# Kernel optimization log

Measured on AMD Instinct MI355X. Metric: run time of the kernel, lower is better.

## Reference

```python
import jax, jax.numpy as jnp
import numpy as np

GROUP_SIZE = 16
MIN_SIGMA = 1e-4


def setup_inputs() -> dict:
    key = jax.random.key(0)
    k1, k2, k3 = jax.random.split(key, 3)
    B, N, M, F = 4, 8192, 4096, 64
    return {
        "point_cloud": jax.random.normal(k1, (B, 3, N), dtype=jnp.float32),
        "query_cloud": jax.random.normal(k2, (B, 3, M), dtype=jnp.float32),
        "point_features": jax.random.normal(k3, (B, F, N), dtype=jnp.float32),
        "temperature": jnp.asarray(1.0, dtype=jnp.float32),
    }


def reference(point_cloud, query_cloud, point_features, temperature):
    # point_cloud: (B,3,N), query_cloud: (B,3,M), point_features: (B,F,N)
    k = GROUP_SIZE
    # Pairwise squared distances (B, M, N): ||q||^2 + ||p||^2 - 2 q.p
    q_sq = jnp.sum(query_cloud ** 2, axis=1)              # (B, M)
    p_sq = jnp.sum(point_cloud ** 2, axis=1)              # (B, N)
    qp = jnp.einsum('bdm,bdn->bmn', query_cloud, point_cloud)
    d2 = q_sq[:, :, None] + p_sq[:, None, :] - 2.0 * qp   # (B, M, N)
    # k nearest neighbors per query
    _, idx = jax.lax.top_k(-d2, k)                         # (B, M, k)

    # Gather neighbor coords and features: (B, 3, M, k), (B, F, M, k)
    idx_b = idx[:, None, :, :]                             # (B,1,M,k)
    grouped_points = jnp.take_along_axis(
        point_cloud[:, :, None, :], jnp.broadcast_to(idx_b, (idx.shape[0], 3, idx.shape[1], k)), axis=3)
    grouped_features = jnp.take_along_axis(
        point_features[:, :, None, :],
        jnp.broadcast_to(idx_b, (idx.shape[0], point_features.shape[1], idx.shape[1], k)), axis=3)

    # Soft-projection weights
    sigma = jnp.maximum(temperature ** 2, jnp.asarray(MIN_SIGMA, dtype=temperature.dtype))
    deltas = grouped_points - query_cloud[:, :, :, None]   # (B,3,M,k)
    dist = jnp.sum(deltas ** 2, axis=1, keepdims=True) / sigma  # (B,1,M,k)
    weights = jax.nn.softmax(-dist, axis=3)                # (B,1,M,k)

    projected_points = jnp.sum(grouped_points * weights, axis=3)     # (B,3,M)
    propagated_features = jnp.sum(grouped_features * weights, axis=3)  # (B,F,M)
    return (projected_points, propagated_features)
```

## Files before the change

kernel.cpp:

```cpp
#include <hip/hip_runtime.h>


#define BB 4
#define NN 8192
#define MM 4096
#define FF 64
#define KK 16
#define CHUNK 2048
#define NCHUNK 4
#define QPW 4
#define QPB 32
#define SCAP 54
#define NTHR 1024
#define STG 33

__device__ __forceinline__ float min3f(float a, float b, float c) {
    float d;
    asm("v_min3_f32 %0, %1, %2, %3" : "=v"(d) : "v"(a), "v"(b), "v"(c));
    return d;
}

__global__ __launch_bounds__(256) void transpose_feat(const float* __restrict__ pf,
                                                      float* __restrict__ pfT) {
    __shared__ float tile[64][65];
    const int b = blockIdx.y;
    const int n0 = blockIdx.x * 64;
    const int t = threadIdx.x;
    const int n = t & 63, fq = t >> 6;
#pragma unroll
    for (int i = 0; i < 16; ++i) {
        int f = fq * 16 + i;
        tile[f][n] = pf[(size_t)b * FF * NN + (size_t)f * NN + n0 + n];
    }
    __syncthreads();
    const int f2 = t & 63, nq = t >> 6;
#pragma unroll
    for (int i = 0; i < 16; ++i) {
        int nn2 = nq * 16 + i;
        pfT[(size_t)b * NN * FF + (size_t)(n0 + nn2) * FF + f2] = tile[f2][nn2];
    }
}

__device__ __forceinline__ unsigned mapf(float f) {
    unsigned u = __float_as_uint(f);
    return (u & 0x80000000u) ? ~u : (u | 0x80000000u);
}
__device__ __forceinline__ float unmapf(unsigned k) {
    return (k & 0x80000000u) ? __uint_as_float(k ^ 0x80000000u)
                             : __uint_as_float(~k);
}

#define STAGE(C)                                                            \
    do {                                                                    \
        if (t < CHUNK / 4) {                                                \
            int base_ = (C)*CHUNK + t * 4;                                  \
            float4 x4_ = *(const float4*)(pcb + base_);                     \
            float4 y4_ = *(const float4*)(pcb + NN + base_);                \
            float4 z4_ = *(const float4*)(pcb + 2 * NN + base_);            \
            *(float4*)(s_pts + t * 4) = x4_;                                \
            *(float4*)(s_pts + CHUNK + t * 4) = y4_;                        \
            *(float4*)(s_pts + 2 * CHUNK + t * 4) = z4_;                    \
            float4 p4_;                                                     \
            p4_.x = fmaf(x4_.x, x4_.x, fmaf(y4_.x, y4_.x, z4_.x * z4_.x));  \
            p4_.y = fmaf(x4_.y, x4_.y, fmaf(y4_.y, y4_.y, z4_.y * z4_.y));  \
            p4_.z = fmaf(x4_.z, x4_.z, fmaf(y4_.z, y4_.z, z4_.z * z4_.z));  \
            p4_.w = fmaf(x4_.w, x4_.w, fmaf(y4_.w, y4_.w, z4_.w * z4_.w));  \
            *(float4*)(s_pts + 3 * CHUNK + t * 4) = p4_;                    \
        }                                                                   \
    } while (0)

#define VAL(X, Y, Z, PS, QX, QY, QZ) \
    fmaf((X), (QX), fmaf((Y), (QY), fmaf((Z), (QZ), (PS))))

#define PUSH(WQ, V, I)                                          \
    do {                                                        \
        int pos_ = atomicAdd(&s_cnt[WQ], 1);                    \
        if (pos_ < SCAP) {                                      \
            s_surv[((WQ)*SCAP + pos_) * 2] = (V);               \
            s_surv[((WQ)*SCAP + pos_) * 2 + 1] = __int_as_float(I); \
        }                                                       \
    } while (0)

__global__ __launch_bounds__(NTHR, 8) void soft_proj_kernel(
    const float* __restrict__ pc, const float* __restrict__ qc,
    const float* __restrict__ pf, const float* __restrict__ pfT,
    const float* __restrict__ temp, float* __restrict__ out, int useT) {
    __shared__ __align__(16) float s_pts[4 * CHUNK];
    __shared__ __align__(16) float s_surv[QPB * SCAP * 2];
    __shared__ int s_cnt[QPB];
    __shared__ int s_sel[QPB * KK];
    __shared__ float s_thr[2 * QPB];

    const int bid = blockIdx.x;
    const int b = bid >> 7;
    const int m0 = (bid & 127) * QPB;
    const int t = threadIdx.x;
    const int wave = t >> 6;
    const int lane = t & 63;
    const int pairIdx = wave & 7;
    const int half = wave >> 3;

    const float* pcb = pc + (size_t)b * 3 * NN;
    const float* qcb = qc + (size_t)b * 3 * MM;

    float qx2[QPW], qy2[QPW], qz2[QPW];
#pragma unroll
    for (int q = 0; q < QPW; ++q) {
        int m = m0 + pairIdx * QPW + q;
        qx2[q] = -2.0f * qcb[m];
        qy2[q] = -2.0f * qcb[MM + m];
        qz2[q] = -2.0f * qcb[2 * MM + m];
    }

    float mnA[QPW], mnB[QPW];
#pragma unroll
    for (int q = 0; q < QPW; ++q) { mnA[q] = 3.0e38f; mnB[q] = 3.0e38f; }

    for (int c = 0; c < NCHUNK; ++c) {
        __syncthreads();
        STAGE(c);
        __syncthreads();
        const int ob = half * 1024 + lane * 4;
#pragma unroll
        for (int g = 0; g < 4; ++g) {
            int oo = ob + g * 256;
            float4 x4 = *(const float4*)(s_pts + oo);
            float4 y4 = *(const float4*)(s_pts + CHUNK + oo);
            float4 z4 = *(const float4*)(s_pts + 2 * CHUNK + oo);
            float4 p4 = *(const float4*)(s_pts + 3 * CHUNK + oo);
#pragma unroll
            for (int q = 0; q < QPW; ++q) {
                float v0 = VAL(x4.x, y4.x, z4.x, p4.x, qx2[q], qy2[q], qz2[q]);
                float v1 = VAL(x4.y, y4.y, z4.y, p4.y, qx2[q], qy2[q], qz2[q]);
                float v2 = VAL(x4.z, y4.z, z4.z, p4.z, qx2[q], qy2[q], qz2[q]);
                float v3 = VAL(x4.w, y4.w, z4.w, p4.w, qx2[q], qy2[q], qz2[q]);
                mnA[q] = min3f(v0, v1, mnA[q]);
                mnB[q] = min3f(v2, v3, mnB[q]);
            }
        }
    }

#pragma unroll
    for (int q = 0; q < QPW; ++q) {
        unsigned key = mapf(fminf(mnA[q], mnB[q]));
        unsigned res = 0u;
        for (int bb = 31; bb >= 16; --bb) {
            unsigned cand = res | (1u << bb);
            unsigned long long bal = __ballot(key < cand);
            int c2 = __popcll(bal);
            if (c2 < 8) res = cand;
        }
        if (lane == 0)
            s_thr[half * QPB + pairIdx * QPW + q] = unmapf(res | 0xFFFFu);
    }
    if (t < QPB) s_cnt[t] = 0;
    __syncthreads();

    const int qo = (wave >> 2) * 8;
    const int qtr = wave & 3;
    float qx2b[8], qy2b[8], qz2b[8], thv[8];
#pragma unroll
    for (int q = 0; q < 8; ++q) {
        int m = m0 + qo + q;
        qx2b[q] = -2.0f * qcb[m];
        qy2b[q] = -2.0f * qcb[MM + m];
        qz2b[q] = -2.0f * qcb[2 * MM + m];
        thv[q] = fmaxf(s_thr[qo + q], s_thr[QPB + qo + q]);
    }

    for (int c = 0; c < NCHUNK; ++c) {
        __syncthreads();
        STAGE(c);
        __syncthreads();
        const int ob = qtr * 512 + lane * 4;
#pragma unroll
        for (int g = 0; g < 2; ++g) {
            int oo = ob + g * 256;
            float4 x4 = *(const float4*)(s_pts + oo);
            float4 y4 = *(const float4*)(s_pts + CHUNK + oo);
            float4 z4 = *(const float4*)(s_pts + 2 * CHUNK + oo);
            float4 p4 = *(const float4*)(s_pts + 3 * CHUNK + oo);
            int gi = c * CHUNK + oo;
#pragma unroll
            for (int q = 0; q < 8; ++q) {
                float v0 = VAL(x4.x, y4.x, z4.x, p4.x, qx2b[q], qy2b[q], qz2b[q]);
                float v1 = VAL(x4.y, y4.y, z4.y, p4.y, qx2b[q], qy2b[q], qz2b[q]);
                float v2 = VAL(x4.z, y4.z, z4.z, p4.z, qx2b[q], qy2b[q], qz2b[q]);
                float v3 = VAL(x4.w, y4.w, z4.w, p4.w, qx2b[q], qy2b[q], qz2b[q]);
                if (fminf(min3f(v0, v1, v2), v3) <= thv[q]) {
                    int wqq = qo + q;
                    if (v0 <= thv[q]) PUSH(wqq, v0, gi + 0);
                    if (v1 <= thv[q]) PUSH(wqq, v1, gi + 1);
                    if (v2 <= thv[q]) PUSH(wqq, v2, gi + 2);
                    if (v3 <= thv[q]) PUSH(wqq, v3, gi + 3);
                }
            }
        }
    }
    __syncthreads();

#pragma unroll
    for (int qq = 0; qq < 2; ++qq) {
        int wq = wave * 2 + qq;
        int cnt = s_cnt[wq];
        cnt = __builtin_amdgcn_readfirstlane(cnt);
        if (cnt > SCAP) cnt = SCAP;
        bool valid = lane < cnt;
        float mv = 0.f;
        int mi = 0;
        if (valid) {
            mv = s_surv[(wq * SCAP + lane) * 2];
            mi = __float_as_int(s_surv[(wq * SCAP + lane) * 2 + 1]);
        }
        int rank = 0;
        for (int j = 0; j < cnt; ++j) {
            float vj = s_surv[(wq * SCAP + j) * 2];
            int ij = __float_as_int(s_surv[(wq * SCAP + j) * 2 + 1]);
            if (valid && (vj < mv || (vj == mv && ij < mi))) rank++;
        }
        if (valid && rank < KK) s_sel[wq * KK + rank] = mi;
    }
    __syncthreads();

    float* stage = s_surv;
    float tval = temp[0];
    float sigma = fmaxf(tval * tval, 1.0e-4f);
    float inv_sigma = 1.0f / sigma;
    const float* pfTb = pfT + (size_t)b * NN * FF;
    const float* pfb = pf + (size_t)b * FF * NN;

#pragma unroll
    for (int qq = 0; qq < 2; ++qq) {
        int wq = wave * 2 + qq;
        int m = m0 + wq;
        float qxe = qcb[m], qye = qcb[MM + m], qze = qcb[2 * MM + m];
        int ik = s_sel[wq * KK + (lane & 15)];
        float px = pcb[ik], py = pcb[NN + ik], pz = pcb[2 * NN + ik];
        float dx = px - qxe, dy = py - qye, dz = pz - qze;
        float dk = fmaf(dx, dx, fmaf(dy, dy, dz * dz));
        float dmin = dk;
#pragma unroll
        for (int s = 1; s < 16; s <<= 1) dmin = fminf(dmin, __shfl_xor(dmin, s));
        float e = __expf((dmin - dk) * inv_sigma);
        float ssum = e;
#pragma unroll
        for (int s = 1; s < 16; s <<= 1) ssum += __shfl_xor(ssum, s);
        float w = e * (1.0f / ssum);
        float sx = w * px, sy = w * py, sz = w * pz;
#pragma unroll
        for (int s = 1; s < 16; s <<= 1) {
            sx += __shfl_xor(sx, s);
            sy += __shfl_xor(sy, s);
            sz += __shfl_xor(sz, s);
        }
        float facc = 0.f;
#pragma unroll
        for (int k = 0; k < KK; ++k) {
            float wk = __shfl(w, k);
            int iik = __shfl(ik, k);
            float fv = useT ? pfTb[(size_t)iik * FF + lane]
                            : pfb[(size_t)lane * NN + iik];
            facc = fmaf(wk, fv, facc);
        }
        stage[lane * STG + wq] = facc;
        if (lane == 0) {
            stage[(64) * STG + wq] = sx;
            stage[(65) * STG + wq] = sy;
            stage[(66) * STG + wq] = sz;
        }
    }
    __syncthreads();

    const size_t featOff = (size_t)BB * 3 * MM;
    for (int j = t; j < 67 * QPB; j += NTHR) {
        int row = j >> 5, col = j & 31;
        float v = stage[row * STG + col];
        int m = m0 + col;
        if (row < 64)
            out[featOff + (size_t)b * FF * MM + (size_t)row * MM + m] = v;
        else
            out[(size_t)b * 3 * MM + (size_t)(row - 64) * MM + m] = v;
    }
}

extern "C" void kernel_launch(void* const* d_in, const int* in_sizes, int n_in,
                              void* d_out, int out_size, void* d_ws, size_t ws_size,
                              hipStream_t stream) {
    (void)in_sizes; (void)n_in; (void)out_size;
    const float* pc = (const float*)d_in[0];
    const float* qc = (const float*)d_in[1];
    const float* pf = (const float*)d_in[2];
    const float* temp = (const float*)d_in[3];
    float* out = (float*)d_out;
    float* pfT = (float*)d_ws;
    const size_t needT = (size_t)BB * NN * FF * sizeof(float);
    int useT = (ws_size >= needT && d_ws != nullptr) ? 1 : 0;

    if (useT) {
        hipLaunchKernelGGL(transpose_feat, dim3(NN / 64, BB), dim3(256), 0, stream,
                           pf, pfT);
    }
    hipLaunchKernelGGL(soft_proj_kernel, dim3((BB * MM) / QPB), dim3(NTHR), 0,
                       stream, pc, qc, pf, pfT, temp, out, useT);
}
```

Baseline: 137.0 us.

## Stage full-width point chunks and reuse pass-one query mapping in survivor pass

Doubles the shared-memory chunk to 4096 points so all 1024 threads stage data, halving the number of staging rounds and barriers in both passes. The second (survivor-collection) pass now reuses the first pass's query-to-wave mapping and register-held query coordinates, so the extra loads and the 8-query layout are gone. s_sel is aliased onto s_pts to offset the larger shared buffer. The trade-off is more LDS per block, which may lower occupancy, and fewer queries per wave in pass two, which means more shared-memory point reads per query.

```diff
diff --git a/kernel.cpp b/kernel.cpp
--- a/kernel.cpp
+++ b/kernel.cpp
@@ -6,8 +6,8 @@
 #define MM 4096
 #define FF 64
 #define KK 16
-#define CHUNK 2048
-#define NCHUNK 4
+#define CHUNK 4096
+#define NCHUNK 2
 #define QPW 4
 #define QPB 32
 #define SCAP 54
@@ -52,21 +52,19 @@
 
 #define STAGE(C)                                                            \
     do {                                                                    \
-        if (t < CHUNK / 4) {                                                \
-            int base_ = (C)*CHUNK + t * 4;                                  \
-            float4 x4_ = *(const float4*)(pcb + base_);                     \
-            float4 y4_ = *(const float4*)(pcb + NN + base_);                \
-            float4 z4_ = *(const float4*)(pcb + 2 * NN + base_);            \
-            *(float4*)(s_pts + t * 4) = x4_;                                \
-            *(float4*)(s_pts + CHUNK + t * 4) = y4_;                        \
-            *(float4*)(s_pts + 2 * CHUNK + t * 4) = z4_;                    \
-            float4 p4_;                                                     \
-            p4_.x = fmaf(x4_.x, x4_.x, fmaf(y4_.x, y4_.x, z4_.x * z4_.x));  \
-            p4_.y = fmaf(x4_.y, x4_.y, fmaf(y4_.y, y4_.y, z4_.y * z4_.y));  \
-            p4_.z = fmaf(x4_.z, x4_.z, fmaf(y4_.z, y4_.z, z4_.z * z4_.z));  \
-            p4_.w = fmaf(x4_.w, x4_.w, fmaf(y4_.w, y4_.w, z4_.w * z4_.w));  \
-            *(float4*)(s_pts + 3 * CHUNK + t * 4) = p4_;                    \
-        }                                                                   \
+        int base_ = (C)*CHUNK + t * 4;                                      \
+        float4 x4_ = *(const float4*)(pcb + base_);                         \
+        float4 y4_ = *(const float4*)(pcb + NN + base_);                    \
+        float4 z4_ = *(const float4*)(pcb + 2 * NN + base_);                \
+        *(float4*)(s_pts + t * 4) = x4_;                                    \
+        *(float4*)(s_pts + CHUNK + t * 4) = y4_;                            \
+        *(float4*)(s_pts + 2 * CHUNK + t * 4) = z4_;                        \
+        float4 p4_;                                                         \
+        p4_.x = fmaf(x4_.x, x4_.x, fmaf(y4_.x, y4_.x, z4_.x * z4_.x));      \
+        p4_.y = fmaf(x4_.y, x4_.y, fmaf(y4_.y, y4_.y, z4_.y * z4_.y));      \
+        p4_.z = fmaf(x4_.z, x4_.z, fmaf(y4_.z, y4_.z, z4_.z * z4_.z));      \
+        p4_.w = fmaf(x4_.w, x4_.w, fmaf(y4_.w, y4_.w, z4_.w * z4_.w));      \
+        *(float4*)(s_pts + 3 * CHUNK + t * 4) = p4_;                        \
     } while (0)
 
 #define VAL(X, Y, Z, PS, QX, QY, QZ) \
@@ -88,8 +86,8 @@
     __shared__ __align__(16) float s_pts[4 * CHUNK];
     __shared__ __align__(16) float s_surv[QPB * SCAP * 2];
     __shared__ int s_cnt[QPB];
-    __shared__ int s_sel[QPB * KK];
     __shared__ float s_thr[2 * QPB];
+    int* s_sel = (int*)s_pts;
 
     const int bid = blockIdx.x;
     const int b = bid >> 7;
@@ -120,9 +118,9 @@
         __syncthreads();
         STAGE(c);
         __syncthreads();
-        const int ob = half * 1024 + lane * 4;
-#pragma unroll
-        for (int g = 0; g < 4; ++g) {
+        const int ob = half * 2048 + lane * 4;
+#pragma unroll
+        for (int g = 0; g < 8; ++g) {
             int oo = ob + g * 256;
             float4 x4 = *(const float4*)(s_pts + oo);
             float4 y4 = *(const float4*)(s_pts + CHUNK + oo);
@@ -155,26 +153,18 @@
     }
     if (t < QPB) s_cnt[t] = 0;
     __syncthreads();
-
-    const int qo = (wave >> 2) * 8;
-    const int qtr = wave & 3;
-    float qx2b[8], qy2b[8], qz2b[8], thv[8];
-#pragma unroll
-    for (int q = 0; q < 8; ++q) {
-        int m = m0 + qo + q;
-        qx2b[q] = -2.0f * qcb[m];
-        qy2b[q] = -2.0f * qcb[MM + m];
-        qz2b[q] = -2.0f * qcb[2 * MM + m];
-        thv[q] = fmaxf(s_thr[qo + q], s_thr[QPB + qo + q]);
-    }
+    float thv[QPW];
+#pragma unroll
+    for (int q = 0; q < QPW; ++q)
+        thv[q] = fmaxf(s_thr[pairIdx * QPW + q], s_thr[QPB + pairIdx * QPW + q]);
 
     for (int c = 0; c < NCHUNK; ++c) {
         __syncthreads();
         STAGE(c);
         __syncthreads();
-        const int ob = qtr * 512 + lane * 4;
-#pragma unroll
-        for (int g = 0; g < 2; ++g) {
+        const int ob = half * 2048 + lane * 4;
+#pragma unroll
+        for (int g = 0; g < 8; ++g) {
             int oo = ob + g * 256;
             float4 x4 = *(const float4*)(s_pts + oo);
             float4 y4 = *(const float4*)(s_pts + CHUNK + oo);
@@ -182,13 +172,13 @@
             float4 p4 = *(const float4*)(s_pts + 3 * CHUNK + oo);
             int gi = c * CHUNK + oo;
 #pragma unroll
-            for (int q = 0; q < 8; ++q) {
-                float v0 = VAL(x4.x, y4.x, z4.x, p4.x, qx2b[q], qy2b[q], qz2b[q]);
-                float v1 = VAL(x4.y, y4.y, z4.y, p4.y, qx2b[q], qy2b[q], qz2b[q]);
-                float v2 = VAL(x4.z, y4.z, z4.z, p4.z, qx2b[q], qy2b[q], qz2b[q]);
-                float v3 = VAL(x4.w, y4.w, z4.w, p4.w, qx2b[q], qy2b[q], qz2b[q]);
+            for (int q = 0; q < QPW; ++q) {
+                float v0 = VAL(x4.x, y4.x, z4.x, p4.x, qx2[q], qy2[q], qz2[q]);
+                float v1 = VAL(x4.y, y4.y, z4.y, p4.y, qx2[q], qy2[q], qz2[q]);
+                float v2 = VAL(x4.z, y4.z, z4.z, p4.z, qx2[q], qy2[q], qz2[q]);
+                float v3 = VAL(x4.w, y4.w, z4.w, p4.w, qx2[q], qy2[q], qz2[q]);
                 if (fminf(min3f(v0, v1, v2), v3) <= thv[q]) {
-                    int wqq = qo + q;
+                    int wqq = pairIdx * QPW + q;
                     if (v0 <= thv[q]) PUSH(wqq, v0, gi + 0);
                     if (v1 <= thv[q]) PUSH(wqq, v1, gi + 1);
                     if (v2 <= thv[q]) PUSH(wqq, v2, gi + 2);
```

Measured after the change: 119.3 us. 1.15x faster.
